# Kernel optimization log

Hardware: AMD Instinct MI355X
Metric: run time of the kernel (lower is better)

The kernel has to match this reference:

```python
import jax, jax.numpy as jnp
import numpy as np
import math

NH = 8   # num heads
DH = 64  # d_head = 512/8
D = 512
L = 6

def _pe(seq, d):
    pos = np.arange(seq, dtype=np.float32)[:, None]
    div = np.exp(np.arange(0, d, 2, dtype=np.float32) * (-math.log(10000.0) / d))
    pe = np.zeros((seq, d), dtype=np.float32)
    pe[:, 0::2] = np.sin(pos * div)
    pe[:, 1::2] = np.cos(pos * div)
    return jnp.asarray(pe)

def _ln(x, g, b, eps=1e-6):
    m = x.mean(-1, keepdims=True)
    v = ((x - m) ** 2).mean(-1, keepdims=True)  # unbiased=False
    return g * (x - m) / jnp.sqrt(v + eps) + b

def _mha(q_in, k_in, v_in, qkv_w, qkv_b, o_w, o_b, mask):
    b, sq, d = q_in.shape
    sk = k_in.shape[1]
    q = (q_in @ qkv_w[0] + qkv_b[0]).reshape(b, sq, NH, DH).transpose(0, 2, 1, 3)  # [b,h,sq,dh]
    k = (k_in @ qkv_w[1] + qkv_b[1]).reshape(b, sk, NH, DH).transpose(0, 2, 1, 3)
    v = (v_in @ qkv_w[2] + qkv_b[2]).reshape(b, sk, NH, DH).transpose(0, 2, 1, 3)
    scores = jnp.einsum('bhqd,bhkd->bhqk', q, k) / math.sqrt(DH)  # [b,h,sq,sk]
    if mask is not None:
        scores = jnp.where(mask, -jnp.inf, scores)  # mask True = masked, broadcast over b,h
    w = jax.nn.softmax(scores, axis=-1)
    out = jnp.einsum('bhqk,bhkd->bhqd', w, v).transpose(0, 2, 1, 3).reshape(b, sq, d)
    return out @ o_w + o_b

def _ff(x, w1, b1, w2, b2):
    return jax.nn.relu(x @ w1 + b1) @ w2 + b2

def reference(src, tgt, src_emb, tgt_emb,
              enc_qkv_w, enc_qkv_b, enc_o_w, enc_o_b,
              enc_ff_w1, enc_ff_b1, enc_ff_w2, enc_ff_b2,
              enc_ln_g, enc_ln_b, enc_fg, enc_fb,
              dec_sqkv_w, dec_sqkv_b, dec_so_w, dec_so_b,
              dec_cqkv_w, dec_cqkv_b, dec_co_w, dec_co_b,
              dec_ff_w1, dec_ff_b1, dec_ff_w2, dec_ff_b2,
              dec_ln_g, dec_ln_b, dec_fg, dec_fb):
    S, T = src.shape[1], tgt.shape[1]
    scale = math.sqrt(D)
    # ---- encoder (pre-LN) ----
    x = src_emb[src] * scale + _pe(S, D)  # [b,S,d]
    for i in range(L):
        h = _ln(x, enc_ln_g[i, 0], enc_ln_b[i, 0])
        x = x + _mha(h, h, h, enc_qkv_w[i], enc_qkv_b[i], enc_o_w[i], enc_o_b[i], None)
        h = _ln(x, enc_ln_g[i, 1], enc_ln_b[i, 1])
        x = x + _ff(h, enc_ff_w1[i], enc_ff_b1[i], enc_ff_w2[i], enc_ff_b2[i])
    memory = _ln(x, enc_fg, enc_fb)
    # ---- decoder (pre-LN) ----
    causal = jnp.triu(jnp.ones((T, T), dtype=bool), 1)  # True above diagonal = masked
    y = tgt_emb[tgt] * scale + _pe(T, D)  # [b,T,d]
    for i in range(L):
        h = _ln(y, dec_ln_g[i, 0], dec_ln_b[i, 0])
        y = y + _mha(h, h, h, dec_sqkv_w[i], dec_sqkv_b[i], dec_so_w[i], dec_so_b[i], causal)
        h = _ln(y, dec_ln_g[i, 1], dec_ln_b[i, 1])
        y = y + _mha(h, memory, memory, dec_cqkv_w[i], dec_cqkv_b[i], dec_co_w[i], dec_co_b[i], None)
        h = _ln(y, dec_ln_g[i, 2], dec_ln_b[i, 2])
        y = y + _ff(h, dec_ff_w1[i], dec_ff_b1[i], dec_ff_w2[i], dec_ff_b2[i])
    return _ln(y, dec_fg, dec_fb)

def setup_inputs():
    key = jax.random.key(0)
    ks = iter(jax.random.split(key, 40))
    B, S, T, V, DFF = 8, 128, 128, 32000, 2048
    s = 0.02
    inp = {
        'src': jax.random.randint(next(ks), (B, S), 0, V, dtype=jnp.int32),
        'tgt': jax.random.randint(next(ks), (B, T), 0, V, dtype=jnp.int32),
        'src_emb': jax.random.normal(next(ks), (V, D), jnp.float32) * s,
        'tgt_emb': jax.random.normal(next(ks), (V, D), jnp.float32) * s,
        'enc_qkv_w': jax.random.normal(next(ks), (L, 3, D, D), jnp.float32) * s,
        'enc_qkv_b': jnp.zeros((L, 3, D), jnp.float32),
        'enc_o_w': jax.random.normal(next(ks), (L, D, D), jnp.float32) * s,
        'enc_o_b': jnp.zeros((L, D), jnp.float32),
        'enc_ff_w1': jax.random.normal(next(ks), (L, D, DFF), jnp.float32) * s,
        'enc_ff_b1': jnp.zeros((L, DFF), jnp.float32),
        'enc_ff_w2': jax.random.normal(next(ks), (L, DFF, D), jnp.float32) * s,
        'enc_ff_b2': jnp.zeros((L, D), jnp.float32),
        'enc_ln_g': jnp.ones((L, 2, D), jnp.float32),
        'enc_ln_b': jnp.zeros((L, 2, D), jnp.float32),
        'enc_fg': jnp.ones((D,), jnp.float32),
        'enc_fb': jnp.zeros((D,), jnp.float32),
        'dec_sqkv_w': jax.random.normal(next(ks), (L, 3, D, D), jnp.float32) * s,
        'dec_sqkv_b': jnp.zeros((L, 3, D), jnp.float32),
        'dec_so_w': jax.random.normal(next(ks), (L, D, D), jnp.float32) * s,
        'dec_so_b': jnp.zeros((L, D), jnp.float32),
        'dec_cqkv_w': jax.random.normal(next(ks), (L, 3, D, D), jnp.float32) * s,
        'dec_cqkv_b': jnp.zeros((L, 3, D), jnp.float32),
        'dec_co_w': jax.random.normal(next(ks), (L, D, D), jnp.float32) * s,
        'dec_co_b': jnp.zeros((L, D), jnp.float32),
        'dec_ff_w1': jax.random.normal(next(ks), (L, D, DFF), jnp.float32) * s,
        'dec_ff_b1': jnp.zeros((L, DFF), jnp.float32),
        'dec_ff_w2': jax.random.normal(next(ks), (L, DFF, D), jnp.float32) * s,
        'dec_ff_b2': jnp.zeros((L, D), jnp.float32),
        'dec_ln_g': jnp.ones((L, 3, D), jnp.float32),
        'dec_ln_b': jnp.zeros((L, 3, D), jnp.float32),
        'dec_fg': jnp.ones((D,), jnp.float32),
        'dec_fb': jnp.zeros((D,), jnp.float32),
    }
    return inp
```

## Files before the change

kernel.cpp:

```cpp
#include <hip/hip_runtime.h>
#include <hip/hip_bf16.h>
#include <math.h>

#define D 512
#define NH 8
#define DHEAD 64
#define LAYERS 6
#define DFF 2048
#define BATCH 8
#define SEQ 128
#define ROWS (BATCH * SEQ)

typedef float f32x4 __attribute__((ext_vector_type(4)));
typedef short bf16x8 __attribute__((ext_vector_type(8)));

__device__ __forceinline__ unsigned short f2b(float x) {
    return __builtin_bit_cast(unsigned short, __float2bfloat16(x));
}

__global__ __launch_bounds__(256) void embed_pe_kernel(
        const int* __restrict__ tok0, const int* __restrict__ tok1,
        const float* __restrict__ emb0, const float* __restrict__ emb1,
        float* __restrict__ out0, float* __restrict__ out1)
{
    const int z = blockIdx.z;
    const int* tok = z ? tok1 : tok0;
    const float* emb = z ? emb1 : emb0;
    float* out = z ? out1 : out0;
    int i = blockIdx.x * 256 + threadIdx.x;
    int bs = i >> 9;
    int d  = i & 511;
    int s  = bs & (SEQ - 1);
    int tk = tok[bs];
    float dv  = expf(-(float)(d & ~1) * (9.210340371976184f / 512.0f));
    float arg = (float)s * dv;
    float pe  = (d & 1) ? cosf(arg) : sinf(arg);
    out[i] = emb[(size_t)tk * D + d] * 22.627416997969522f + pe;
}

struct TSeg { const float* src; unsigned short* dst; int cnt; };
struct TMulti { TSeg seg[6]; };

__global__ __launch_bounds__(256) void transpose_multi_kernel(TMulti m, int R, int C)
{
    __shared__ float t[32][33];
    int z = blockIdx.z, s = 0;
    while (z >= m.seg[s].cnt) { z -= m.seg[s].cnt; ++s; }
    const float* src = m.seg[s].src + (size_t)z * R * C;
    unsigned short* dst = m.seg[s].dst + (size_t)z * R * C;
    const int r0 = blockIdx.y << 5, c0 = blockIdx.x << 5;
    const int tid = threadIdx.x;
    const int rr = tid >> 3, cc = (tid & 7) << 2;
    float4 v = *(const float4*)(src + (size_t)(r0 + rr) * C + c0 + cc);
    t[rr][cc] = v.x; t[rr][cc + 1] = v.y; t[rr][cc + 2] = v.z; t[rr][cc + 3] = v.w;
    __syncthreads();
    const int oc = tid >> 3, or4 = (tid & 7) << 2;
    ushort4 o;
    o.x = f2b(t[or4 + 0][oc]);
    o.y = f2b(t[or4 + 1][oc]);
    o.z = f2b(t[or4 + 2][oc]);
    o.w = f2b(t[or4 + 3][oc]);
    *(ushort4*)(dst + (size_t)(c0 + oc) * R + r0 + or4) = o;
}

template<int OUT_BF16>
__global__ __launch_bounds__(256) void ln_kernel(const float* __restrict__ x,
        const float* __restrict__ g, const float* __restrict__ bta,
        void* __restrict__ outp)
{
    int lane = threadIdx.x & 63;
    int row  = (blockIdx.x << 2) + (threadIdx.x >> 6);
    const float* xr = x + (size_t)row * D;
    int c = lane * 8;
    float4 v0 = *(const float4*)(xr + c);
    float4 v1 = *(const float4*)(xr + c + 4);
    float s  = v0.x + v0.y + v0.z + v0.w + v1.x + v1.y + v1.z + v1.w;
    float sq = v0.x*v0.x + v0.y*v0.y + v0.z*v0.z + v0.w*v0.w
             + v1.x*v1.x + v1.y*v1.y + v1.z*v1.z + v1.w*v1.w;
    #pragma unroll
    for (int o = 32; o; o >>= 1) {
        s  += __shfl_xor(s, o);
        sq += __shfl_xor(sq, o);
    }
    float mean = s * (1.0f / D);
    float var  = sq * (1.0f / D) - mean * mean;
    float inv  = rsqrtf(var + 1e-6f);
    float4 g0 = *(const float4*)(g + c),   g1 = *(const float4*)(g + c + 4);
    float4 b0 = *(const float4*)(bta + c), b1 = *(const float4*)(bta + c + 4);
    float4 o0, o1;
    o0.x = g0.x * (v0.x - mean) * inv + b0.x;
    o0.y = g0.y * (v0.y - mean) * inv + b0.y;
    o0.z = g0.z * (v0.z - mean) * inv + b0.z;
    o0.w = g0.w * (v0.w - mean) * inv + b0.w;
    o1.x = g1.x * (v1.x - mean) * inv + b1.x;
    o1.y = g1.y * (v1.y - mean) * inv + b1.y;
    o1.z = g1.z * (v1.z - mean) * inv + b1.z;
    o1.w = g1.w * (v1.w - mean) * inv + b1.w;
    if (OUT_BF16) {
        unsigned short* orow = (unsigned short*)outp + (size_t)row * D + c;
        uint4 o;
        o.x = (unsigned int)f2b(o0.x) | ((unsigned int)f2b(o0.y) << 16);
        o.y = (unsigned int)f2b(o0.z) | ((unsigned int)f2b(o0.w) << 16);
        o.z = (unsigned int)f2b(o1.x) | ((unsigned int)f2b(o1.y) << 16);
        o.w = (unsigned int)f2b(o1.z) | ((unsigned int)f2b(o1.w) << 16);
        *(uint4*)orow = o;
    } else {
        float* orow = (float*)outp + (size_t)row * D + c;
        *(float4*)(orow)     = o0;
        *(float4*)(orow + 4) = o1;
    }
}

template<int RESID, int RELU, int OUT_BF16>
__global__ __launch_bounds__(256) void mgemm_kernel(
        const unsigned short* __restrict__ A,
        const unsigned short* __restrict__ Wt,
        const float* __restrict__ bias,
        const float* __restrict__ Rp,
        void* __restrict__ Cout,
        int N, int K,
        long aZ, long wZ, long bZ, long cZ)
{
    __shared__ unsigned short As[2][64][72];
    __shared__ unsigned short Bs[2][64][72];
    const long z = blockIdx.z;
    const unsigned short* Ab = A  + z * aZ;
    const unsigned short* Wb = Wt + z * wZ;
    const float* biasb = bias + z * bZ;
    const int tid  = threadIdx.x;
    const int lane = tid & 63, wid = tid >> 6;
    const int wm = wid >> 1, wn = wid & 1;
    const int bm = blockIdx.y << 6, bn = blockIdx.x << 6;
    const int srow = tid >> 2, sk = (tid & 3) << 4;
    const unsigned short* Ag = Ab + (size_t)(bm + srow) * K + sk;
    const unsigned short* Bg = Wb + (size_t)(bn + srow) * K + sk;
    const int fr = lane & 15;
    const int fk = (lane >> 4) << 3;
    f32x4 acc[2][2];
    #pragma unroll
    for (int i = 0; i < 2; ++i)
        #pragma unroll
        for (int j = 0; j < 2; ++j)
            acc[i][j] = (f32x4){0.f, 0.f, 0.f, 0.f};

    uint4 a0 = *(const uint4*)Ag, a1 = *(const uint4*)(Ag + 8);
    uint4 b0 = *(const uint4*)Bg, b1 = *(const uint4*)(Bg + 8);
    const int T = K >> 6;
    for (int t = 0; t < T; ++t) {
        const int p = t & 1;
        *(uint4*)&As[p][srow][sk]     = a0;
        *(uint4*)&As[p][srow][sk + 8] = a1;
        *(uint4*)&Bs[p][srow][sk]     = b0;
        *(uint4*)&Bs[p][srow][sk + 8] = b1;
        if (t + 1 < T) {
            Ag += 64; Bg += 64;
            a0 = *(const uint4*)Ag; a1 = *(const uint4*)(Ag + 8);
            b0 = *(const uint4*)Bg; b1 = *(const uint4*)(Bg + 8);
        }
        __syncthreads();
        #pragma unroll
        for (int s = 0; s < 2; ++s) {
            bf16x8 af0 = *(const bf16x8*)&As[p][wm * 32 + fr][s * 32 + fk];
            bf16x8 af1 = *(const bf16x8*)&As[p][wm * 32 + 16 + fr][s * 32 + fk];
            bf16x8 bf0 = *(const bf16x8*)&Bs[p][wn * 32 + fr][s * 32 + fk];
            bf16x8 bf1 = *(const bf16x8*)&Bs[p][wn * 32 + 16 + fr][s * 32 + fk];
            acc[0][0] = __builtin_amdgcn_mfma_f32_16x16x32_bf16(af0, bf0, acc[0][0], 0, 0, 0);
            acc[0][1] = __builtin_amdgcn_mfma_f32_16x16x32_bf16(af0, bf1, acc[0][1], 0, 0, 0);
            acc[1][0] = __builtin_amdgcn_mfma_f32_16x16x32_bf16(af1, bf0, acc[1][0], 0, 0, 0);
            acc[1][1] = __builtin_amdgcn_mfma_f32_16x16x32_bf16(af1, bf1, acc[1][1], 0, 0, 0);
        }
    }
    const int cr   = (lane >> 4) << 2;
    const int ccol = lane & 15;
    #pragma unroll
    for (int i = 0; i < 2; ++i)
        #pragma unroll
        for (int j = 0; j < 2; ++j) {
            int col = bn + wn * 32 + j * 16 + ccol;
            float bsv = biasb[col];
            #pragma unroll
            for (int r = 0; r < 4; ++r) {
                int row = bm + wm * 32 + i * 16 + cr + r;
                float v = acc[i][j][r] + bsv;
                if (RESID) v += Rp[(size_t)row * N + col];
                if (RELU)  v = fmaxf(v, 0.f);
                if (OUT_BF16) ((unsigned short*)Cout + z * cZ)[(size_t)row * N + col] = f2b(v);
                else          ((float*)Cout)[(size_t)row * N + col] = v;
            }
        }
}

template<int CAUSAL>
__device__ __forceinline__ void attn_phase(
        const unsigned short* Ks, const unsigned short* Vt,
        const unsigned short* Qs, unsigned short* Ps,
        int qbase, int brow, int hoff, unsigned short* __restrict__ Op,
        int lane, int wid)
{
    const int fr = lane & 15, fg = lane >> 4;
    f32x4 accs[8];
    #pragma unroll
    for (int kf = 0; kf < 8; ++kf) accs[kf] = (f32x4){0.f, 0.f, 0.f, 0.f};
    bf16x8 aq0 = *(const bf16x8*)&Qs[(wid * 16 + fr) * 72 + fg * 8];
    bf16x8 aq1 = *(const bf16x8*)&Qs[(wid * 16 + fr) * 72 + 32 + fg * 8];
    #pragma unroll
    for (int kf = 0; kf < 8; ++kf) {
        bf16x8 bk0 = *(const bf16x8*)&Ks[(kf * 16 + fr) * 72 + fg * 8];
        bf16x8 bk1 = *(const bf16x8*)&Ks[(kf * 16 + fr) * 72 + 32 + fg * 8];
        accs[kf] = __builtin_amdgcn_mfma_f32_16x16x32_bf16(aq0, bk0, accs[kf], 0, 0, 0);
        accs[kf] = __builtin_amdgcn_mfma_f32_16x16x32_bf16(aq1, bk1, accs[kf], 0, 0, 0);
    }
    const float SC = 0.125f * 1.44269504f;
    float linv[4];
    #pragma unroll
    for (int r = 0; r < 4; ++r) {
        int qrow = qbase + wid * 16 + fg * 4 + r;
        float sv[8];
        #pragma unroll
        for (int kf = 0; kf < 8; ++kf) {
            float s = accs[kf][r] * SC;
            if (CAUSAL) {
                int key = kf * 16 + fr;
                if (key > qrow) s = -1e30f;
            }
            sv[kf] = s;
        }
        float m = sv[0];
        #pragma unroll
        for (int kf = 1; kf < 8; ++kf) m = fmaxf(m, sv[kf]);
        #pragma unroll
        for (int o = 1; o < 16; o <<= 1) m = fmaxf(m, __shfl_xor(m, o));
        float l = 0.f;
        #pragma unroll
        for (int kf = 0; kf < 8; ++kf) {
            float p = exp2f(sv[kf] - m);
            l += p;
            Ps[(wid * 16 + fg * 4 + r) * 136 + kf * 16 + fr] = f2b(p);
        }
        #pragma unroll
        for (int o = 1; o < 16; o <<= 1) l += __shfl_xor(l, o);
        linv[r] = 1.f / l;
    }
    f32x4 acco[4];
    #pragma unroll
    for (int df = 0; df < 4; ++df) acco[df] = (f32x4){0.f, 0.f, 0.f, 0.f};
    #pragma unroll
    for (int ks = 0; ks < 4; ++ks) {
        bf16x8 pa = *(const bf16x8*)&Ps[(wid * 16 + fr) * 136 + ks * 32 + fg * 8];
        #pragma unroll
        for (int df = 0; df < 4; ++df) {
            bf16x8 vb = *(const bf16x8*)&Vt[(df * 16 + fr) * 136 + ks * 32 + fg * 8];
            acco[df] = __builtin_amdgcn_mfma_f32_16x16x32_bf16(pa, vb, acco[df], 0, 0, 0);
        }
    }
    #pragma unroll
    for (int df = 0; df < 4; ++df)
        #pragma unroll
        for (int r = 0; r < 4; ++r) {
            int qrow = qbase + wid * 16 + fg * 4 + r;
            Op[(size_t)(brow + qrow) * D + hoff + df * 16 + fr] = f2b(acco[df][r] * linv[r]);
        }
}

template<int CAUSAL>
__global__ __launch_bounds__(256) void attn_kernel(
        const unsigned short* __restrict__ Qp, int qs,
        const unsigned short* __restrict__ Kp,
        const unsigned short* __restrict__ Vp, int kvs,
        unsigned short* __restrict__ Op)
{
    __shared__ unsigned short Ks[128 * 72];
    __shared__ unsigned short Qs[64 * 72];
    __shared__ unsigned short Vt[64 * 136];
    __shared__ unsigned short Ps[64 * 136];
    const int bh    = blockIdx.x >> 1;
    const int qbase = (blockIdx.x & 1) << 6;
    const int brow  = (bh >> 3) * SEQ;
    const int hoff  = (bh & 7) * DHEAD;
    const int tid = threadIdx.x, lane = tid & 63, wid = tid >> 6;

    #pragma unroll
    for (int it = 0; it < 4; ++it) {
        int idx = it * 256 + tid;
        int row = idx >> 3;
        int c8  = (idx & 7) << 3;
        *(uint4*)&Ks[row * 72 + c8] =
            *(const uint4*)(Kp + (size_t)(brow + row) * kvs + hoff + c8);
        uint4 vu = *(const uint4*)(Vp + (size_t)(brow + row) * kvs + hoff + c8);
        unsigned arr[4] = {vu.x, vu.y, vu.z, vu.w};
        #pragma unroll
        for (int j = 0; j < 8; ++j)
            Vt[(c8 + j) * 136 + row] = (unsigned short)(arr[j >> 1] >> ((j & 1) * 16));
    }
    #pragma unroll
    for (int it = 0; it < 2; ++it) {
        int idx = it * 256 + tid;
        int row = idx >> 3;
        int c8  = (idx & 7) << 3;
        *(uint4*)&Qs[row * 72 + c8] =
            *(const uint4*)(Qp + (size_t)(brow + qbase + row) * qs + hoff + c8);
    }
    __syncthreads();
    attn_phase<CAUSAL>(Ks, Vt, Qs, Ps, qbase, brow, hoff, Op, lane, wid);
}

__global__ __launch_bounds__(256) void xattn_kernel(
        const unsigned short* __restrict__ Hb,
        const unsigned short* __restrict__ Wq,
        const float* __restrict__ bias,
        const unsigned short* __restrict__ KV,
        unsigned short* __restrict__ Op)
{
    __shared__ __align__(16) char lds[63488];
    unsigned short* Ks  = (unsigned short*)(lds);
    unsigned short* Vt  = (unsigned short*)(lds + 18432);
    unsigned short* Qs  = (unsigned short*)(lds + 35840);
    unsigned short* Ps  = (unsigned short*)(lds + 46080);
    unsigned short* Hs  = (unsigned short*)(lds + 35840);
    unsigned short* Wqs = (unsigned short*)(lds + 46080);

    const int bh = blockIdx.x >> 1;
    const int qbase = (blockIdx.x & 1) << 6;
    const int h = bh & 7;
    const int brow = (bh >> 3) * SEQ;
    const int hoff = h * DHEAD;
    const int tid = threadIdx.x, lane = tid & 63, wid = tid >> 6;
    const int fr = lane & 15, fg = lane >> 4;

    #pragma unroll
    for (int it = 0; it < 4; ++it) {
        int idx = it * 256 + tid;
        int row = idx >> 3, c8 = (idx & 7) << 3;
        const unsigned short* kvrow = KV + (size_t)(brow + row) * 1024 + hoff;
        *(uint4*)&Ks[row * 72 + c8] = *(const uint4*)(kvrow + c8);
        uint4 vu = *(const uint4*)(kvrow + 512 + c8);
        unsigned arr[4] = {vu.x, vu.y, vu.z, vu.w};
        #pragma unroll
        for (int j = 0; j < 8; ++j)
            Vt[(c8 + j) * 136 + row] = (unsigned short)(arr[j >> 1] >> ((j & 1) * 16));
    }
    f32x4 accQ[4];
    #pragma unroll
    for (int n = 0; n < 4; ++n) accQ[n] = (f32x4){0.f, 0.f, 0.f, 0.f};
    for (int kt = 0; kt < 8; ++kt) {
        #pragma unroll
        for (int it = 0; it < 2; ++it) {
            int idx = it * 256 + tid;
            int row = idx >> 3, c8 = (idx & 7) << 3;
            *(uint4*)&Hs[row * 72 + c8] =
                *(const uint4*)(Hb + (size_t)(brow + qbase + row) * 512 + kt * 64 + c8);
            *(uint4*)&Wqs[row * 72 + c8] =
                *(const uint4*)(Wq + (size_t)(hoff + row) * 512 + kt * 64 + c8);
        }
        __syncthreads();
        #pragma unroll
        for (int s = 0; s < 2; ++s) {
            int fk = s * 32 + fg * 8;
            bf16x8 hq = *(const bf16x8*)&Hs[(wid * 16 + fr) * 72 + fk];
            #pragma unroll
            for (int n = 0; n < 4; ++n) {
                bf16x8 wq = *(const bf16x8*)&Wqs[(n * 16 + fr) * 72 + fk];
                accQ[n] = __builtin_amdgcn_mfma_f32_16x16x32_bf16(hq, wq, accQ[n], 0, 0, 0);
            }
        }
        __syncthreads();
    }
    #pragma unroll
    for (int n = 0; n < 4; ++n) {
        int d = n * 16 + fr;
        float bq = bias[hoff + d];
        #pragma unroll
        for (int r = 0; r < 4; ++r) {
            int ql = wid * 16 + fg * 4 + r;
            Qs[ql * 72 + d] = f2b(accQ[n][r] + bq);
        }
    }
    __syncthreads();
    attn_phase<0>(Ks, Vt, Qs, Ps, qbase, brow, hoff, Op, lane, wid);
}

extern "C" void kernel_launch(void* const* d_in, const int* in_sizes, int n_in,
                              void* d_out, int out_size, void* d_ws, size_t ws_size,
                              hipStream_t stream)
{
    const int*   src       = (const int*)d_in[0];
    const int*   tgt       = (const int*)d_in[1];
    const float* src_emb   = (const float*)d_in[2];
    const float* tgt_emb   = (const float*)d_in[3];
    const float* enc_qkv_w = (const float*)d_in[4];
    const float* enc_qkv_b = (const float*)d_in[5];
    const float* enc_o_w   = (const float*)d_in[6];
    const float* enc_o_b   = (const float*)d_in[7];
    const float* enc_ff_w1 = (const float*)d_in[8];
    const float* enc_ff_b1 = (const float*)d_in[9];
    const float* enc_ff_w2 = (const float*)d_in[10];
    const float* enc_ff_b2 = (const float*)d_in[11];
    const float* enc_ln_g  = (const float*)d_in[12];
    const float* enc_ln_b  = (const float*)d_in[13];
    const float* enc_fg    = (const float*)d_in[14];
    const float* enc_fb    = (const float*)d_in[15];
    const float* dec_sqkv_w = (const float*)d_in[16];
    const float* dec_sqkv_b = (const float*)d_in[17];
    const float* dec_so_w   = (const float*)d_in[18];
    const float* dec_so_b   = (const float*)d_in[19];
    const float* dec_cqkv_w = (const float*)d_in[20];
    const float* dec_cqkv_b = (const float*)d_in[21];
    const float* dec_co_w   = (const float*)d_in[22];
    const float* dec_co_b   = (const float*)d_in[23];
    const float* dec_ff_w1  = (const float*)d_in[24];
    const float* dec_ff_b1  = (const float*)d_in[25];
    const float* dec_ff_w2  = (const float*)d_in[26];
    const float* dec_ff_b2  = (const float*)d_in[27];
    const float* dec_ln_g   = (const float*)d_in[28];
    const float* dec_ln_b   = (const float*)d_in[29];
    const float* dec_fg     = (const float*)d_in[30];
    const float* dec_fb     = (const float*)d_in[31];

    unsigned short* wp = (unsigned short*)d_ws;
    unsigned short* WencQKV  = wp; wp += (size_t)6 * 786432;
    unsigned short* WencO    = wp; wp += (size_t)6 * 262144;
    unsigned short* WencF1   = wp; wp += (size_t)6 * 1048576;
    unsigned short* WencF2   = wp; wp += (size_t)6 * 1048576;
    unsigned short* WdecSQKV = wp; wp += (size_t)6 * 786432;
    unsigned short* WdecSO   = wp; wp += (size_t)6 * 262144;
    unsigned short* WdecCQKV = wp; wp += (size_t)6 * 786432;
    unsigned short* WdecCO   = wp; wp += (size_t)6 * 262144;
    unsigned short* WdecF1   = wp; wp += (size_t)6 * 1048576;
    unsigned short* WdecF2   = wp; wp += (size_t)6 * 1048576;
    unsigned short* Hb   = wp; wp += ROWS * D;
    unsigned short* QKVb = wp; wp += ROWS * 3 * D;
    unsigned short* CKVall = wp; wp += (size_t)6 * ROWS * 1024;
    unsigned short* ATTb = wp; wp += ROWS * D;
    unsigned short* F1b  = wp; wp += ROWS * DFF;
    unsigned short* MEMb = wp; wp += ROWS * D;
    float* X  = (float*)wp;  wp += ROWS * D * 2;
    float* X2 = (float*)wp;  wp += ROWS * D * 2;

    {
        TMulti mA = {{ {enc_qkv_w,  WencQKV,  18},
                       {enc_o_w,    WencO,     6},
                       {dec_sqkv_w, WdecSQKV, 18},
                       {dec_so_w,   WdecSO,    6},
                       {dec_cqkv_w, WdecCQKV, 18},
                       {dec_co_w,   WdecCO,    6} }};
        transpose_multi_kernel<<<dim3(16, 16, 72), 256, 0, stream>>>(mA, 512, 512);
        TMulti mB = {{ {enc_ff_w1, WencF1, 6},
                       {dec_ff_w1, WdecF1, 6},
                       {nullptr, nullptr, 1 << 30}, {nullptr, nullptr, 1 << 30},
                       {nullptr, nullptr, 1 << 30}, {nullptr, nullptr, 1 << 30} }};
        transpose_multi_kernel<<<dim3(64, 16, 12), 256, 0, stream>>>(mB, 512, 2048);
        TMulti mC = {{ {enc_ff_w2, WencF2, 6},
                       {dec_ff_w2, WdecF2, 6},
                       {nullptr, nullptr, 1 << 30}, {nullptr, nullptr, 1 << 30},
                       {nullptr, nullptr, 1 << 30}, {nullptr, nullptr, 1 << 30} }};
        transpose_multi_kernel<<<dim3(16, 64, 12), 256, 0, stream>>>(mC, 2048, 512);
    }

    embed_pe_kernel<<<dim3(2048, 1, 2), 256, 0, stream>>>(src, tgt, src_emb, tgt_emb, X, X2);

    for (int i = 0; i < LAYERS; ++i) {
        ln_kernel<1><<<256, 256, 0, stream>>>(X, enc_ln_g + (size_t)(i*2+0)*D, enc_ln_b + (size_t)(i*2+0)*D, Hb);
        mgemm_kernel<0,0,1><<<dim3(24,16,1), 256, 0, stream>>>(Hb, WencQKV + (size_t)i*786432,
                enc_qkv_b + (size_t)i*1536, nullptr, QKVb, 1536, 512, 0, 0, 0, 0);
        attn_kernel<0><<<128, 256, 0, stream>>>(QKVb, 1536, QKVb + 512, QKVb + 1024, 1536, ATTb);
        mgemm_kernel<1,0,0><<<dim3(8,16,1), 256, 0, stream>>>(ATTb, WencO + (size_t)i*262144,
                enc_o_b + (size_t)i*512, X, X, 512, 512, 0, 0, 0, 0);
        ln_kernel<1><<<256, 256, 0, stream>>>(X, enc_ln_g + (size_t)(i*2+1)*D, enc_ln_b + (size_t)(i*2+1)*D, Hb);
        mgemm_kernel<0,1,1><<<dim3(32,16,1), 256, 0, stream>>>(Hb, WencF1 + (size_t)i*1048576,
                enc_ff_b1 + (size_t)i*DFF, nullptr, F1b, DFF, 512, 0, 0, 0, 0);
        mgemm_kernel<1,0,0><<<dim3(8,16,1), 256, 0, stream>>>(F1b, WencF2 + (size_t)i*1048576,
                enc_ff_b2 + (size_t)i*512, X, X, 512, DFF, 0, 0, 0, 0);
    }
    ln_kernel<1><<<256, 256, 0, stream>>>(X, enc_fg, enc_fb, MEMb);

    mgemm_kernel<0,0,1><<<dim3(16,16,6), 256, 0, stream>>>(MEMb, WdecCQKV + 262144,
            dec_cqkv_b + 512, nullptr, CKVall, 1024, 512,
            0, 786432, 1536, (long)ROWS * 1024);

    for (int i = 0; i < LAYERS; ++i) {
        ln_kernel<1><<<256, 256, 0, stream>>>(X2, dec_ln_g + (size_t)(i*3+0)*D, dec_ln_b + (size_t)(i*3+0)*D, Hb);
        mgemm_kernel<0,0,1><<<dim3(24,16,1), 256, 0, stream>>>(Hb, WdecSQKV + (size_t)i*786432,
                dec_sqkv_b + (size_t)i*1536, nullptr, QKVb, 1536, 512, 0, 0, 0, 0);
        attn_kernel<1><<<128, 256, 0, stream>>>(QKVb, 1536, QKVb + 512, QKVb + 1024, 1536, ATTb);
        mgemm_kernel<1,0,0><<<dim3(8,16,1), 256, 0, stream>>>(ATTb, WdecSO + (size_t)i*262144,
                dec_so_b + (size_t)i*512, X2, X2, 512, 512, 0, 0, 0, 0);
        ln_kernel<1><<<256, 256, 0, stream>>>(X2, dec_ln_g + (size_t)(i*3+1)*D, dec_ln_b + (size_t)(i*3+1)*D, Hb);
        xattn_kernel<<<128, 256, 0, stream>>>(Hb, WdecCQKV + (size_t)i*786432,
                dec_cqkv_b + (size_t)i*1536, CKVall + (size_t)i*ROWS*1024, ATTb);
        mgemm_kernel<1,0,0><<<dim3(8,16,1), 256, 0, stream>>>(ATTb, WdecCO + (size_t)i*262144,
                dec_co_b + (size_t)i*512, X2, X2, 512, 512, 0, 0, 0, 0);
        ln_kernel<1><<<256, 256, 0, stream>>>(X2, dec_ln_g + (size_t)(i*3+2)*D, dec_ln_b + (size_t)(i*3+2)*D, Hb);
        mgemm_kernel<0,1,1><<<dim3(32,16,1), 256, 0, stream>>>(Hb, WdecF1 + (size_t)i*1048576,
                dec_ff_b1 + (size_t)i*DFF, nullptr, F1b, DFF, 512, 0, 0, 0, 0);
        mgemm_kernel<1,0,0><<<dim3(8,16,1), 256, 0, stream>>>(F1b, WdecF2 + (size_t)i*1048576,
                dec_ff_b2 + (size_t)i*512, X2, X2, 512, DFF, 0, 0, 0, 0);
    }
    ln_kernel<0><<<256, 256, 0, stream>>>(X2, dec_fg, dec_fb, d_out);
}
```

Before: 750.4 us.

## Fuse LayerNorm into consuming GEMMs via per-row stats from producer epilogues

Removes the standalone LayerNorm launches by having the residual GEMM epilogues (and the embedding kernel) emit per-row partial sum and sum-of-squares into a small stats buffer. Consuming GEMMs and the cross-attention kernel then read fp32 activations, rebuild mean and rstd from those partials, and apply the norm while staging A tiles into LDS. This saves a kernel launch and a bf16 round trip per norm. In exchange, A loads become fp32 (twice the bytes), every N-tile block recomputes the norm, and E[x²]-mean² variance is less numerically stable.

```diff
diff --git a/kernel.cpp b/kernel.cpp
--- a/kernel.cpp
+++ b/kernel.cpp
@@ -18,15 +18,28 @@
     return __builtin_bit_cast(unsigned short, __float2bfloat16(x));
 }
 
+__device__ __forceinline__ uint4 ln_pack8(float4 x0, float4 x1,
+        float4 g0, float4 g1, float4 e0, float4 e1, float mean, float r)
+{
+    uint4 o;
+    o.x = (unsigned)f2b((x0.x-mean)*r*g0.x+e0.x) | ((unsigned)f2b((x0.y-mean)*r*g0.y+e0.y) << 16);
+    o.y = (unsigned)f2b((x0.z-mean)*r*g0.z+e0.z) | ((unsigned)f2b((x0.w-mean)*r*g0.w+e0.w) << 16);
+    o.z = (unsigned)f2b((x1.x-mean)*r*g1.x+e1.x) | ((unsigned)f2b((x1.y-mean)*r*g1.y+e1.y) << 16);
+    o.w = (unsigned)f2b((x1.z-mean)*r*g1.z+e1.z) | ((unsigned)f2b((x1.w-mean)*r*g1.w+e1.w) << 16);
+    return o;
+}
+
 __global__ __launch_bounds__(256) void embed_pe_kernel(
         const int* __restrict__ tok0, const int* __restrict__ tok1,
         const float* __restrict__ emb0, const float* __restrict__ emb1,
-        float* __restrict__ out0, float* __restrict__ out1)
+        float* __restrict__ out0, float* __restrict__ out1,
+        float2* __restrict__ st0, float2* __restrict__ st1)
 {
     const int z = blockIdx.z;
     const int* tok = z ? tok1 : tok0;
     const float* emb = z ? emb1 : emb0;
     float* out = z ? out1 : out0;
+    float2* st = z ? st1 : st0;
     int i = blockIdx.x * 256 + threadIdx.x;
     int bs = i >> 9;
     int d  = i & 511;
@@ -35,7 +48,27 @@
     float dv  = expf(-(float)(d & ~1) * (9.210340371976184f / 512.0f));
     float arg = (float)s * dv;
     float pe  = (d & 1) ? cosf(arg) : sinf(arg);
-    out[i] = emb[(size_t)tk * D + d] * 22.627416997969522f + pe;
+    float o = emb[(size_t)tk * D + d] * 22.627416997969522f + pe;
+    out[i] = o;
+    float sum = o, sq = o * o;
+    #pragma unroll
+    for (int off = 32; off; off >>= 1) {
+        sum += __shfl_xor(sum, off);
+        sq  += __shfl_xor(sq, off);
+    }
+    __shared__ float ws[4][2];
+    const int lane = threadIdx.x & 63, wid = threadIdx.x >> 6;
+    if (lane == 0) { ws[wid][0] = sum; ws[wid][1] = sq; }
+    __syncthreads();
+    if (threadIdx.x == 0) {
+        float S = ws[0][0] + ws[1][0] + ws[2][0] + ws[3][0];
+        float Q = ws[0][1] + ws[1][1] + ws[2][1] + ws[3][1];
+        int row = bs, slot = blockIdx.x & 1;
+        st[row * 8 + slot] = make_float2(S, Q);
+        if (slot == 0)
+            #pragma unroll
+            for (int k = 2; k < 8; ++k) st[row * 8 + k] = make_float2(0.f, 0.f);
+    }
 }
 
 struct TSeg { const float* src; unsigned short* dst; int cnt; };
@@ -63,10 +96,9 @@
     *(ushort4*)(dst + (size_t)(c0 + oc) * R + r0 + or4) = o;
 }
 
-template<int OUT_BF16>
 __global__ __launch_bounds__(256) void ln_kernel(const float* __restrict__ x,
         const float* __restrict__ g, const float* __restrict__ bta,
-        void* __restrict__ outp)
+        float* __restrict__ outp)
 {
     int lane = threadIdx.x & 63;
     int row  = (blockIdx.x << 2) + (threadIdx.x >> 6);
@@ -96,35 +128,28 @@
     o1.y = g1.y * (v1.y - mean) * inv + b1.y;
     o1.z = g1.z * (v1.z - mean) * inv + b1.z;
     o1.w = g1.w * (v1.w - mean) * inv + b1.w;
-    if (OUT_BF16) {
-        unsigned short* orow = (unsigned short*)outp + (size_t)row * D + c;
-        uint4 o;
-        o.x = (unsigned int)f2b(o0.x) | ((unsigned int)f2b(o0.y) << 16);
-        o.y = (unsigned int)f2b(o0.z) | ((unsigned int)f2b(o0.w) << 16);
-        o.z = (unsigned int)f2b(o1.x) | ((unsigned int)f2b(o1.y) << 16);
-        o.w = (unsigned int)f2b(o1.z) | ((unsigned int)f2b(o1.w) << 16);
-        *(uint4*)orow = o;
-    } else {
-        float* orow = (float*)outp + (size_t)row * D + c;
-        *(float4*)(orow)     = o0;
-        *(float4*)(orow + 4) = o1;
-    }
-}
-
-template<int RESID, int RELU, int OUT_BF16>
+    float* orow = outp + (size_t)row * D + c;
+    *(float4*)(orow)     = o0;
+    *(float4*)(orow + 4) = o1;
+}
+
+template<int RESID, int RELU, int OUT_BF16, int LNA, int STATS>
 __global__ __launch_bounds__(256) void mgemm_kernel(
-        const unsigned short* __restrict__ A,
+        const void* __restrict__ Aptr,
         const unsigned short* __restrict__ Wt,
         const float* __restrict__ bias,
         const float* __restrict__ Rp,
         void* __restrict__ Cout,
         int N, int K,
-        long aZ, long wZ, long bZ, long cZ)
+        long wZ, long bZ, long cZ,
+        const float* __restrict__ lng, const float* __restrict__ lnb,
+        const float2* __restrict__ stIn, float2* __restrict__ stOut)
 {
     __shared__ unsigned short As[2][64][72];
     __shared__ unsigned short Bs[2][64][72];
+    __shared__ float lnM[64], lnR[64];
+    __shared__ float sred[64][2][2];
     const long z = blockIdx.z;
-    const unsigned short* Ab = A  + z * aZ;
     const unsigned short* Wb = Wt + z * wZ;
     const float* biasb = bias + z * bZ;
     const int tid  = threadIdx.x;
@@ -132,10 +157,31 @@
     const int wm = wid >> 1, wn = wid & 1;
     const int bm = blockIdx.y << 6, bn = blockIdx.x << 6;
     const int srow = tid >> 2, sk = (tid & 3) << 4;
-    const unsigned short* Ag = Ab + (size_t)(bm + srow) * K + sk;
-    const unsigned short* Bg = Wb + (size_t)(bn + srow) * K + sk;
     const int fr = lane & 15;
     const int fk = (lane >> 4) << 3;
+
+    if (LNA) {
+        if (tid < 64) {
+            const float2* sp = stIn + (size_t)(bm + tid) * 8;
+            float s = 0.f, q = 0.f;
+            #pragma unroll
+            for (int k = 0; k < 8; ++k) { float2 v = sp[k]; s += v.x; q += v.y; }
+            float mean = s * (1.f / 512.f);
+            float var  = q * (1.f / 512.f) - mean * mean;
+            lnM[tid] = mean;
+            lnR[tid] = rsqrtf(var + 1e-6f);
+        }
+        __syncthreads();
+    }
+    const float m_s = LNA ? lnM[srow] : 0.f;
+    const float r_s = LNA ? lnR[srow] : 0.f;
+
+    const unsigned short* Ag = nullptr;
+    const float* Agf = nullptr;
+    if (LNA) Agf = (const float*)Aptr + (size_t)(bm + srow) * 512 + sk;
+    else     Ag  = (const unsigned short*)Aptr + (size_t)(bm + srow) * K + sk;
+    const unsigned short* Bg = Wb + (size_t)(bn + srow) * K + sk;
+
     f32x4 acc[2][2];
     #pragma unroll
     for (int i = 0; i < 2; ++i)
@@ -143,18 +189,42 @@
         for (int j = 0; j < 2; ++j)
             acc[i][j] = (f32x4){0.f, 0.f, 0.f, 0.f};
 
-    uint4 a0 = *(const uint4*)Ag, a1 = *(const uint4*)(Ag + 8);
+    uint4 a0, a1;
+    float4 x0, x1, x2, x3;
+    if (LNA) {
+        x0 = *(const float4*)Agf;       x1 = *(const float4*)(Agf + 4);
+        x2 = *(const float4*)(Agf + 8); x3 = *(const float4*)(Agf + 12);
+    } else {
+        a0 = *(const uint4*)Ag; a1 = *(const uint4*)(Ag + 8);
+    }
     uint4 b0 = *(const uint4*)Bg, b1 = *(const uint4*)(Bg + 8);
     const int T = K >> 6;
     for (int t = 0; t < T; ++t) {
         const int p = t & 1;
-        *(uint4*)&As[p][srow][sk]     = a0;
-        *(uint4*)&As[p][srow][sk + 8] = a1;
+        if (LNA) {
+            const int k0 = t * 64 + sk;
+            float4 g0 = *(const float4*)(lng + k0),     g1 = *(const float4*)(lng + k0 + 4);
+            float4 g2 = *(const float4*)(lng + k0 + 8), g3 = *(const float4*)(lng + k0 + 12);
+            float4 e0 = *(const float4*)(lnb + k0),     e1 = *(const float4*)(lnb + k0 + 4);
+            float4 e2 = *(const float4*)(lnb + k0 + 8), e3 = *(const float4*)(lnb + k0 + 12);
+            *(uint4*)&As[p][srow][sk]     = ln_pack8(x0, x1, g0, g1, e0, e1, m_s, r_s);
+            *(uint4*)&As[p][srow][sk + 8] = ln_pack8(x2, x3, g2, g3, e2, e3, m_s, r_s);
+        } else {
+            *(uint4*)&As[p][srow][sk]     = a0;
+            *(uint4*)&As[p][srow][sk + 8] = a1;
+        }
         *(uint4*)&Bs[p][srow][sk]     = b0;
         *(uint4*)&Bs[p][srow][sk + 8] = b1;
         if (t + 1 < T) {
-            Ag += 64; Bg += 64;
-            a0 = *(const uint4*)Ag; a1 = *(const uint4*)(Ag + 8);
+            Bg += 64;
+            if (LNA) {
+                Agf += 64;
+                x0 = *(const float4*)Agf;       x1 = *(const float4*)(Agf + 4);
+                x2 = *(const float4*)(Agf + 8); x3 = *(const float4*)(Agf + 12);
+            } else {
+                Ag += 64;
+                a0 = *(const uint4*)Ag; a1 = *(const uint4*)(Ag + 8);
+            }
             b0 = *(const uint4*)Bg; b1 = *(const uint4*)(Bg + 8);
         }
         __syncthreads();
@@ -172,6 +242,7 @@
     }
     const int cr   = (lane >> 4) << 2;
     const int ccol = lane & 15;
+    float sl[2][4] = {}, ql[2][4] = {};
     #pragma unroll
     for (int i = 0; i < 2; ++i)
         #pragma unroll
@@ -184,10 +255,35 @@
                 float v = acc[i][j][r] + bsv;
                 if (RESID) v += Rp[(size_t)row * N + col];
                 if (RELU)  v = fmaxf(v, 0.f);
+                if (STATS) { sl[i][r] += v; ql[i][r] += v * v; }
                 if (OUT_BF16) ((unsigned short*)Cout + z * cZ)[(size_t)row * N + col] = f2b(v);
                 else          ((float*)Cout)[(size_t)row * N + col] = v;
             }
         }
+    if (STATS) {
+        #pragma unroll
+        for (int i = 0; i < 2; ++i)
+            #pragma unroll
+            for (int r = 0; r < 4; ++r) {
+                float s = sl[i][r], q = ql[i][r];
+                #pragma unroll
+                for (int o = 1; o < 16; o <<= 1) {
+                    s += __shfl_xor(s, o);
+                    q += __shfl_xor(q, o);
+                }
+                if (fr == 0) {
+                    int lrow = wm * 32 + i * 16 + cr + r;
+                    sred[lrow][wn][0] = s;
+                    sred[lrow][wn][1] = q;
+                }
+            }
+        __syncthreads();
+        if (tid < 64) {
+            float s = sred[tid][0][0] + sred[tid][1][0];
+            float q = sred[tid][0][1] + sred[tid][1][1];
+            stOut[(size_t)(bm + tid) * 8 + blockIdx.x] = make_float2(s, q);
+        }
+    }
 }
 
 template<int CAUSAL>
@@ -305,9 +401,11 @@
 }
 
 __global__ __launch_bounds__(256) void xattn_kernel(
-        const unsigned short* __restrict__ Hb,
+        const float* __restrict__ X2,
         const unsigned short* __restrict__ Wq,
         const float* __restrict__ bias,
+        const float* __restrict__ lng, const float* __restrict__ lnb,
+        const float2* __restrict__ stIn,
         const unsigned short* __restrict__ KV,
         unsigned short* __restrict__ Op)
 {
@@ -318,6 +416,7 @@
     unsigned short* Ps  = (unsigned short*)(lds + 46080);
     unsigned short* Hs  = (unsigned short*)(lds + 35840);
     unsigned short* Wqs = (unsigned short*)(lds + 46080);
+    __shared__ float lnM[64], lnR[64];
 
     const int bh = blockIdx.x >> 1;
     const int qbase = (blockIdx.x & 1) << 6;
@@ -327,6 +426,16 @@
     const int tid = threadIdx.x, lane = tid & 63, wid = tid >> 6;
     const int fr = lane & 15, fg = lane >> 4;
 
+    if (tid < 64) {
+        const float2* sp = stIn + (size_t)(brow + qbase + tid) * 8;
+        float s = 0.f, q = 0.f;
+        #pragma unroll
+        for (int k = 0; k < 8; ++k) { float2 v = sp[k]; s += v.x; q += v.y; }
+        float mean = s * (1.f / 512.f);
+        float var  = q * (1.f / 512.f) - mean * mean;
+        lnM[tid] = mean;
+        lnR[tid] = rsqrtf(var + 1e-6f);
+    }
     #pragma unroll
     for (int it = 0; it < 4; ++it) {
         int idx = it * 256 + tid;
@@ -339,6 +448,7 @@
         for (int j = 0; j < 8; ++j)
             Vt[(c8 + j) * 136 + row] = (unsigned short)(arr[j >> 1] >> ((j & 1) * 16));
     }
+    __syncthreads();
     f32x4 accQ[4];
     #pragma unroll
     for (int n = 0; n < 4; ++n) accQ[n] = (f32x4){0.f, 0.f, 0.f, 0.f};
@@ -347,8 +457,11 @@
         for (int it = 0; it < 2; ++it) {
             int idx = it * 256 + tid;
             int row = idx >> 3, c8 = (idx & 7) << 3;
-            *(uint4*)&Hs[row * 72 + c8] =
-                *(const uint4*)(Hb + (size_t)(brow + qbase + row) * 512 + kt * 64 + c8);
+            const float* xr = X2 + (size_t)(brow + qbase + row) * 512 + kt * 64 + c8;
+            float4 x0 = *(const float4*)xr, x1 = *(const float4*)(xr + 4);
+            float4 g0 = *(const float4*)(lng + kt * 64 + c8), g1 = *(const float4*)(lng + kt * 64 + c8 + 4);
+            float4 e0 = *(const float4*)(lnb + kt * 64 + c8), e1 = *(const float4*)(lnb + kt * 64 + c8 + 4);
+            *(uint4*)&Hs[row * 72 + c8] = ln_pack8(x0, x1, g0, g1, e0, e1, lnM[row], lnR[row]);
             *(uint4*)&Wqs[row * 72 + c8] =
                 *(const uint4*)(Wq + (size_t)(hoff + row) * 512 + kt * 64 + c8);
         }
@@ -427,14 +540,14 @@
     unsigned short* WdecCO   = wp; wp += (size_t)6 * 262144;
     unsigned short* WdecF1   = wp; wp += (size_t)6 * 1048576;
     unsigned short* WdecF2   = wp; wp += (size_t)6 * 1048576;
-    unsigned short* Hb   = wp; wp += ROWS * D;
     unsigned short* QKVb = wp; wp += ROWS * 3 * D;
     unsigned short* CKVall = wp; wp += (size_t)6 * ROWS * 1024;
     unsigned short* ATTb = wp; wp += ROWS * D;
     unsigned short* F1b  = wp; wp += ROWS * DFF;
-    unsigned short* MEMb = wp; wp += ROWS * D;
-    float* X  = (float*)wp;  wp += ROWS * D * 2;
-    float* X2 = (float*)wp;  wp += ROWS * D * 2;
+    float* X   = (float*)wp;  wp += ROWS * D * 2;
+    float* X2  = (float*)wp;  wp += ROWS * D * 2;
+    float2* stX  = (float2*)wp; wp += ROWS * 8 * 4;
+    float2* stX2 = (float2*)wp; wp += ROWS * 8 * 4;
 
     {
         TMulti mA = {{ {enc_qkv_w,  WencQKV,  18},
@@ -456,44 +569,55 @@
         transpose_multi_kernel<<<dim3(16, 64, 12), 256, 0, stream>>>(mC, 2048, 512);
     }
 
-    embed_pe_kernel<<<dim3(2048, 1, 2), 256, 0, stream>>>(src, tgt, src_emb, tgt_emb, X, X2);
+    embed_pe_kernel<<<dim3(2048, 1, 2), 256, 0, stream>>>(src, tgt, src_emb, tgt_emb,
+            X, X2, stX, stX2);
 
     for (int i = 0; i < LAYERS; ++i) {
-        ln_kernel<1><<<256, 256, 0, stream>>>(X, enc_ln_g + (size_t)(i*2+0)*D, enc_ln_b + (size_t)(i*2+0)*D, Hb);
-        mgemm_kernel<0,0,1><<<dim3(24,16,1), 256, 0, stream>>>(Hb, WencQKV + (size_t)i*786432,
-                enc_qkv_b + (size_t)i*1536, nullptr, QKVb, 1536, 512, 0, 0, 0, 0);
+        mgemm_kernel<0,0,1,1,0><<<dim3(24,16,1), 256, 0, stream>>>(X,
+                WencQKV + (size_t)i*786432, enc_qkv_b + (size_t)i*1536, nullptr, QKVb,
+                1536, 512, 0, 0, 0,
+                enc_ln_g + (size_t)(i*2+0)*D, enc_ln_b + (size_t)(i*2+0)*D, stX, nullptr);
         attn_kernel<0><<<128, 256, 0, stream>>>(QKVb, 1536, QKVb + 512, QKVb + 1024, 1536, ATTb);
-        mgemm_kernel<1,0,0><<<dim3(8,16,1), 256, 0, stream>>>(ATTb, WencO + (size_t)i*262144,
-                enc_o_b + (size_t)i*512, X, X, 512, 512, 0, 0, 0, 0);
-        ln_kernel<1><<<256, 256, 0, stream>>>(X, enc_ln_g + (size_t)(i*2+1)*D, enc_ln_b + (size_t)(i*2+1)*D, Hb);
-        mgemm_kernel<0,1,1><<<dim3(32,16,1), 256, 0, stream>>>(Hb, WencF1 + (size_t)i*1048576,
-                enc_ff_b1 + (size_t)i*DFF, nullptr, F1b, DFF, 512, 0, 0, 0, 0);
-        mgemm_kernel<1,0,0><<<dim3(8,16,1), 256, 0, stream>>>(F1b, WencF2 + (size_t)i*1048576,
-                enc_ff_b2 + (size_t)i*512, X, X, 512, DFF, 0, 0, 0, 0);
-    }
-    ln_kernel<1><<<256, 256, 0, stream>>>(X, enc_fg, enc_fb, MEMb);
-
-    mgemm_kernel<0,0,1><<<dim3(16,16,6), 256, 0, stream>>>(MEMb, WdecCQKV + 262144,
-            dec_cqkv_b + 512, nullptr, CKVall, 1024, 512,
-            0, 786432, 1536, (long)ROWS * 1024);
+        mgemm_kernel<1,0,0,0,1><<<dim3(8,16,1), 256, 0, stream>>>(ATTb,
+                WencO + (size_t)i*262144, enc_o_b + (size_t)i*512, X, X,
+                512, 512, 0, 0, 0, nullptr, nullptr, nullptr, stX);
+        mgemm_kernel<0,1,1,1,0><<<dim3(32,16,1), 256, 0, stream>>>(X,
+                WencF1 + (size_t)i*1048576, enc_ff_b1 + (size_t)i*DFF, nullptr, F1b,
+                DFF, 512, 0, 0, 0,
+                enc_ln_g + (size_t)(i*2+1)*D, enc_ln_b + (size_t)(i*2+1)*D, stX, nullptr);
+        mgemm_kernel<1,0,0,0,1><<<dim3(8,16,1), 256, 0, stream>>>(F1b,
+                WencF2 + (size_t)i*1048576, enc_ff_b2 + (size_t)i*512, X, X,
+                512, DFF, 0, 0, 0, nullptr, nullptr, nullptr, stX);
+    }
+
+    mgemm_kernel<0,0,1,1,0><<<dim3(16,16,6), 256, 0, stream>>>(X,
+            WdecCQKV + 262144, dec_cqkv_b + 512, nullptr, CKVall,
+            1024, 512, 786432, 1536, (long)ROWS * 1024,
+            enc_fg, enc_fb, stX, nullptr);
 
     for (int i = 0; i < LAYERS; ++i) {
-        ln_kernel<1><<<256, 256, 0, stream>>>(X2, dec_ln_g + (size_t)(i*3+0)*D, dec_ln_b + (size_t)(i*3+0)*D, Hb);
-        mgemm_kernel<0,0,1><<<dim3(24,16,1), 256, 0, stream>>>(Hb, WdecSQKV + (size_t)i*786432,
-                dec_sqkv_b + (size_t)i*1536, nullptr, QKVb, 1536, 512, 0, 0, 0, 0);
+        mgemm_kernel<0,0,1,1,0><<<dim3(24,16,1), 256, 0, stream>>>(X2,
+                WdecSQKV + (size_t)i*786432, dec_sqkv_b + (size_t)i*1536, nullptr, QKVb,
+                1536, 512, 0, 0, 0,
+                dec_ln_g + (size_t)(i*3+0)*D, dec_ln_b + (size_t)(i*3+0)*D, stX2, nullptr);
         attn_kernel<1><<<128, 256, 0, stream>>>(QKVb, 1536, QKVb + 512, QKVb + 1024, 1536, ATTb);
-        mgemm_kernel<1,0,0><<<dim3(8,16,1), 256, 0, stream>>>(ATTb, WdecSO + (size_t)i*262144,
-                dec_so_b + (size_t)i*512, X2, X2, 512, 512, 0, 0, 0, 0);
-        ln_kernel<1><<<256, 256, 0, stream>>>(X2, dec_ln_g + (size_t)(i*3+1)*D, dec_ln_b + (size_t)(i*3+1)*D, Hb);
-        xattn_kernel<<<128, 256, 0, stream>>>(Hb, WdecCQKV + (size_t)i*786432,
-                dec_cqkv_b + (size_t)i*1536, CKVall + (size_t)i*ROWS*1024, ATTb);
-        mgemm_kernel<1,0,0><<<dim3(8,16,1), 256, 0, stream>>>(ATTb, WdecCO + (size_t)i*262144,
-                dec_co_b + (size_t)i*512, X2, X2, 512, 512, 0, 0, 0, 0);
-        ln_kernel<1><<<256, 256, 0, stream>>>(X2, dec_ln_g + (size_t)(i*3+2)*D, dec_ln_b + (size_t)(i*3+2)*D, Hb);
-        mgemm_kernel<0,1,1><<<dim3(32,16,1), 256, 0, stream>>>(Hb, WdecF1 + (size_t)i*1048576,
-                dec_ff_b1 + (size_t)i*DFF, nullptr, F1b, DFF, 512, 0, 0, 0, 0);
-        mgemm_kernel<1,0,0><<<dim3(8,16,1), 256, 0, stream>>>(F1b, WdecF2 + (size_t)i*1048576,
-                dec_ff_b2 + (size_t)i*512, X2, X2, 512, DFF, 0, 0, 0, 0);
-    }
-    ln_kernel<0><<<256, 256, 0, stream>>>(X2, dec_fg, dec_fb, d_out);
-}
+        mgemm_kernel<1,0,0,0,1><<<dim3(8,16,1), 256, 0, stream>>>(ATTb,
+                WdecSO + (size_t)i*262144, dec_so_b + (size_t)i*512, X2, X2,
+                512, 512, 0, 0, 0, nullptr, nullptr, nullptr, stX2);
+        xattn_kernel<<<128, 256, 0, stream>>>(X2, WdecCQKV + (size_t)i*786432,
+                dec_cqkv_b + (size_t)i*1536,
+                dec_ln_g + (size_t)(i*3+1)*D, dec_ln_b + (size_t)(i*3+1)*D, stX2,
+                CKVall + (size_t)i*ROWS*1024, ATTb);
+        mgemm_kernel<1,0,0,0,1><<<dim3(8,16,1), 256, 0, stream>>>(ATTb,
+                WdecCO + (size_t)i*262144, dec_co_b + (size_t)i*512, X2, X2,
+                512, 512, 0, 0, 0, nullptr, nullptr, nullptr, stX2);
+        mgemm_kernel<0,1,1,1,0><<<dim3(32,16,1), 256, 0, stream>>>(X2,
+                WdecF1 + (size_t)i*1048576, dec_ff_b1 + (size_t)i*DFF, nullptr, F1b,
+                DFF, 512, 0, 0, 0,
+                dec_ln_g + (size_t)(i*3+2)*D, dec_ln_b + (size_t)(i*3+2)*D, stX2, nullptr);
+        mgemm_kernel<1,0,0,0,1><<<dim3(8,16,1), 256, 0, stream>>>(F1b,
+                WdecF2 + (size_t)i*1048576, dec_ff_b2 + (size_t)i*512, X2, X2,
+                512, DFF, 0, 0, 0, nullptr, nullptr, nullptr, stX2);
+    }
+    ln_kernel<<<256, 256, 0, stream>>>(X2, dec_fg, dec_fb, (float*)d_out);
+}
```

Result: slower. 964.1 us (+28.5%).
